# Optimization experiments

Measured on AMD Instinct MI355X. Metric: run time of the kernel, lower is better.

Reference implementation:

```python
import jax, jax.numpy as jnp
import numpy as np

N_BINS = 15


def setup_inputs() -> dict:
    key = jax.random.key(0)
    k1, k2 = jax.random.split(key)
    B, C = 4, 4
    spatial = (128, 128, 128)
    logits = jax.random.normal(k1, (B, C) + spatial, dtype=jnp.float32)
    labels = jax.random.randint(k2, (B, 1) + spatial, 0, C, dtype=jnp.int64)
    return {"logits": logits, "labels": labels}


def _hl1_ace(logits, labels, n_bins=N_BINS):
    B, C = logits.shape[0], logits.shape[1]
    probs = jax.nn.softmax(logits, axis=1) if C > 1 else logits
    # one-hot target (B, C, *spatial)
    target = jax.nn.one_hot(labels[:, 0], C, axis=1, dtype=jnp.float32)
    p = probs.reshape(B, C, -1).astype(jnp.float32)   # (B, C, N)
    t = target.reshape(B, C, -1)                       # (B, C, N)

    eps = jnp.finfo(jnp.float32).eps
    boundaries = jnp.linspace(0.0, 1.0 + eps, n_bins + 1)
    # torch.bucketize(p, boundaries[1:], right=False) == searchsorted side='left'
    bin_idx = jnp.searchsorted(boundaries[1:], p, side="left")  # (B, C, N)

    # fused histogram across all (b, c) slices via one segment_sum
    offsets = (jnp.arange(B * C, dtype=bin_idx.dtype) * n_bins).reshape(B, C, 1)
    seg = (bin_idx + offsets).reshape(-1)
    nseg = B * C * n_bins
    counts = jax.ops.segment_sum(jnp.ones(seg.shape, jnp.float32), seg, num_segments=nseg).reshape(B, C, n_bins)
    sum_p = jax.ops.segment_sum(p.reshape(-1), seg, num_segments=nseg).reshape(B, C, n_bins)
    sum_t = jax.ops.segment_sum(t.reshape(-1), seg, num_segments=nseg).reshape(B, C, n_bins)

    valid = counts > 0
    denom = jnp.where(valid, counts, 1.0)
    mean_p = sum_p / denom
    mean_t = sum_t / denom
    # nanmean over bins: average |mean_p - mean_t| over non-empty bins only
    diff = jnp.where(valid, jnp.abs(mean_p - mean_t), 0.0)
    n_valid = jnp.maximum(valid.sum(-1), 1)
    ace_per_bc = diff.sum(-1) / n_valid.astype(jnp.float32)  # (B, C)

    non_empty = (t.sum(-1) > 0).astype(jnp.float32)          # (B, C)
    return (ace_per_bc * non_empty).mean()


def reference(logits, labels):
    return _hl1_ace(logits, labels)
```

## Files before the change

### kernel.cpp

```cpp
#include <hip/hip_runtime.h>

#define NVOX 2097152u
#define NBINS 15
#define NSEG 240

#if __has_builtin(__builtin_amdgcn_exp2f)
#define EXP2F(x) __builtin_amdgcn_exp2f(x)
#else
#define EXP2F(x) exp2f(x)
#endif
#if __has_builtin(__builtin_amdgcn_rcpf)
#define RCPF(x) __builtin_amdgcn_rcpf(x)
#else
#define RCPF(x) (1.0f / (x))
#endif

__global__ __launch_bounds__(256)
void ace_zero(unsigned* __restrict__ ws) {
    int i = blockIdx.x * 256 + threadIdx.x;
    if (i < 3 * NSEG) ws[i] = 0u;
}

__global__ __launch_bounds__(256, 8)
void ace_hist(const float* __restrict__ logits,
              const int*   __restrict__ labels,
              unsigned* __restrict__ g_cnt,
              unsigned* __restrict__ g_cntt,
              float*    __restrict__ g_sump)
{
    __shared__ unsigned s_hist[60][64];
    __shared__ unsigned s_tab[3][60];

    const int tid  = threadIdx.x;
    const int lane = tid & 63;

    #pragma unroll
    for (int i = 0; i < 15; ++i) ((unsigned*)s_hist)[tid + i * 256] = 0u;
    if (tid < 180) ((unsigned*)s_tab)[tid] = 0u;
    __syncthreads();

    const unsigned b   = (unsigned)blockIdx.x >> 9;
    const unsigned tib = ((unsigned)blockIdx.x & 511u) * 256u + (unsigned)tid;

    const float step  = (1.0f + 1.1920929e-7f) / 15.0f;
    const float scale = 15.0f / (1.0f + 1.1920929e-7f);
    const float LOG2E = 1.44269504088896340736f;

    const float* lbase   = logits + (unsigned long long)(b * 4u) * NVOX;
    const int*   labbase = labels + (unsigned long long)b * NVOX;

    for (int i = 0; i < 4; ++i) {
        const unsigned s = (tib + (unsigned)i * 131072u) << 2;

        const int4 lv4 = *(const int4*)(labbase + s);
        const int lab[4] = { lv4.x, lv4.y, lv4.z, lv4.w };

        const float4 L0 = *(const float4*)(lbase + s);
        const float4 L1 = *(const float4*)(lbase + NVOX + s);
        const float4 L2 = *(const float4*)(lbase + 2u * NVOX + s);
        const float4 L3 = *(const float4*)(lbase + 3u * NVOX + s);

        #pragma unroll
        for (int v = 0; v < 4; ++v) {
            const float e0 = EXP2F((&L0.x)[v] * LOG2E);
            const float e1 = EXP2F((&L1.x)[v] * LOG2E);
            const float e2 = EXP2F((&L2.x)[v] * LOG2E);
            const float e3 = EXP2F((&L3.x)[v] * LOG2E);
            const float inv = RCPF(e0 + e1 + e2 + e3);
            const float pr[4] = { e0 * inv, e1 * inv, e2 * inv, e3 * inv };
            const int lv = lab[v];

            #pragma unroll
            for (int c = 0; c < 4; ++c) {
                const float pv = pr[c];
                int bin = (int)(pv * scale);
                bin = bin > 14 ? 14 : bin;
                if (bin < 14 && step * (float)(bin + 1) < pv) ++bin;
                if (bin > 0 && !(step * (float)bin < pv)) --bin;

                const unsigned qt  = (unsigned)fmaf(pv, 4095.0f, 262144.5f);
                const unsigned inc = qt | ((lv == c) ? 0x2000000u : 0u);
                atomicAdd(&s_hist[c * NBINS + bin][lane], inc);
            }
        }
    }
    __syncthreads();

    if (tid < 240) {
        const int r = tid >> 2, q = tid & 3;
        unsigned sq = 0, sc = 0, st = 0;
        #pragma unroll
        for (int j = 0; j < 16; ++j) {
            const unsigned x = s_hist[r][q * 16 + ((j + r) & 15)];
            sq += x & 0x3FFFFu;
            sc += (x >> 18) & 0x7Fu;
            st += x >> 25;
        }
        atomicAdd(&s_tab[0][r], sq);
        atomicAdd(&s_tab[1][r], sc);
        atomicAdd(&s_tab[2][r], st);
    }
    __syncthreads();

    if (tid < 60) {
        const int gi = (int)(b * 60u) + tid;
        atomicAdd(g_cnt  + gi, s_tab[1][tid]);
        atomicAdd(g_cntt + gi, s_tab[2][tid]);
        atomicAdd(g_sump + gi, (float)s_tab[0][tid] * (1.0f / 4095.0f));
    }
}

__global__ __launch_bounds__(64)
void ace_final(const unsigned* __restrict__ g_cnt,
               const unsigned* __restrict__ g_cntt,
               const float*    __restrict__ g_sump,
               float* __restrict__ out)
{
    const int lane = threadIdx.x;
    float contrib = 0.0f;
    if (lane < 16) {
        float diff_sum = 0.0f;
        int   nvalid   = 0;
        unsigned tot_t = 0u;
        for (int k = 0; k < NBINS; ++k) {
            const int i = lane * NBINS + k;
            const unsigned c  = g_cnt[i];
            const unsigned ct = g_cntt[i];
            const float    sp = g_sump[i];
            tot_t += ct;
            if (c > 0u) {
                const float invc = 1.0f / (float)c;
                diff_sum += fabsf(sp * invc - (float)ct * invc);
                ++nvalid;
            }
        }
        const float ace = diff_sum / (float)(nvalid > 0 ? nvalid : 1);
        contrib = (tot_t > 0u) ? ace : 0.0f;
    }
    #pragma unroll
    for (int off = 32; off > 0; off >>= 1)
        contrib += __shfl_xor(contrib, off, 64);
    if (lane == 0) out[0] = contrib * (1.0f / 16.0f);
}

extern "C" void kernel_launch(void* const* d_in, const int* in_sizes, int n_in,
                              void* d_out, int out_size, void* d_ws, size_t ws_size,
                              hipStream_t stream) {
    const float* logits = (const float*)d_in[0];
    const int*   labels = (const int*)d_in[1];

    unsigned* g_cnt  = (unsigned*)d_ws;
    unsigned* g_cntt = g_cnt + NSEG;
    float*    g_sump = (float*)(g_cntt + NSEG);
    float*    out    = (float*)d_out;

    ace_zero<<<3, 256, 0, stream>>>((unsigned*)d_ws);
    ace_hist<<<2048, 256, 0, stream>>>(logits, labels, g_cnt, g_cntt, g_sump);
    ace_final<<<1, 64, 0, stream>>>(g_cnt, g_cntt, g_sump, out);
}
```

Before: 55.50 us.

## Issue all loads up front per thread and drop exact bin boundary correction

Each thread now handles 16 contiguous voxels, with every label and logit float4 load issued before any compute. This raises memory-level parallelism, and the launch bound drops to 4 waves per SIMD to leave room for the extra registers. The boundary fix-up that matched searchsorted exactly is removed, so binning relies only on truncating p*scale. That can misbin values sitting on a boundary, and the contiguous per-thread layout changes the coalescing pattern.

New measurement: 56.69 us. +2.1%, slower.

```diff
diff --git a/kernel.cpp b/kernel.cpp
--- a/kernel.cpp
+++ b/kernel.cpp
@@ -21,7 +21,38 @@
     if (i < 3 * NSEG) ws[i] = 0u;
 }
 
-__global__ __launch_bounds__(256, 8)
+__device__ __forceinline__ void process4(const int4 lv4,
+                                         const float4 L0, const float4 L1,
+                                         const float4 L2, const float4 L3,
+                                         unsigned (*s_hist)[64], const int lane)
+{
+    const float scale = 15.0f / (1.0f + 1.1920929e-7f);
+    const float LOG2E = 1.44269504088896340736f;
+    const int lab[4] = { lv4.x, lv4.y, lv4.z, lv4.w };
+
+    #pragma unroll
+    for (int v = 0; v < 4; ++v) {
+        const float e0 = EXP2F((&L0.x)[v] * LOG2E);
+        const float e1 = EXP2F((&L1.x)[v] * LOG2E);
+        const float e2 = EXP2F((&L2.x)[v] * LOG2E);
+        const float e3 = EXP2F((&L3.x)[v] * LOG2E);
+        const float inv = RCPF(e0 + e1 + e2 + e3);
+        const float pr[4] = { e0 * inv, e1 * inv, e2 * inv, e3 * inv };
+        const int lv = lab[v];
+
+        #pragma unroll
+        for (int c = 0; c < 4; ++c) {
+            const float pv = pr[c];
+            const int bin = (int)(pv * scale);
+
+            const unsigned qt  = (unsigned)fmaf(pv, 4095.0f, 262144.5f);
+            const unsigned inc = qt | ((lv == c) ? 0x2000000u : 0u);
+            atomicAdd(&s_hist[c * NBINS + bin][lane], inc);
+        }
+    }
+}
+
+__global__ __launch_bounds__(256, 4)
 void ace_hist(const float* __restrict__ logits,
               const int*   __restrict__ labels,
               unsigned* __restrict__ g_cnt,
@@ -41,49 +72,29 @@
 
     const unsigned b   = (unsigned)blockIdx.x >> 9;
     const unsigned tib = ((unsigned)blockIdx.x & 511u) * 256u + (unsigned)tid;
+    const unsigned v0  = tib << 4;
 
-    const float step  = (1.0f + 1.1920929e-7f) / 15.0f;
-    const float scale = 15.0f / (1.0f + 1.1920929e-7f);
-    const float LOG2E = 1.44269504088896340736f;
+    const float* p0 = logits + (unsigned long long)(b * 4u) * NVOX + v0;
+    const int*   ap = labels + (unsigned long long)b * NVOX + v0;
 
-    const float* lbase   = logits + (unsigned long long)(b * 4u) * NVOX;
-    const int*   labbase = labels + (unsigned long long)b * NVOX;
+    int4 lv[4];
+    #pragma unroll
+    for (int j = 0; j < 4; ++j) lv[j] = *(const int4*)(ap + 4 * j);
 
-    for (int i = 0; i < 4; ++i) {
-        const unsigned s = (tib + (unsigned)i * 131072u) << 2;
+    float4 L0[4], L1[4], L2[4], L3[4];
+    #pragma unroll
+    for (int j = 0; j < 4; ++j) L0[j] = *(const float4*)(p0 + 4 * j);
+    #pragma unroll
+    for (int j = 0; j < 4; ++j) L1[j] = *(const float4*)(p0 + NVOX + 4 * j);
+    #pragma unroll
+    for (int j = 0; j < 4; ++j) L2[j] = *(const float4*)(p0 + 2u * NVOX + 4 * j);
+    #pragma unroll
+    for (int j = 0; j < 4; ++j) L3[j] = *(const float4*)(p0 + 3u * NVOX + 4 * j);
 
-        const int4 lv4 = *(const int4*)(labbase + s);
-        const int lab[4] = { lv4.x, lv4.y, lv4.z, lv4.w };
+    #pragma unroll
+    for (int j = 0; j < 4; ++j)
+        process4(lv[j], L0[j], L1[j], L2[j], L3[j], s_hist, lane);
 
-        const float4 L0 = *(const float4*)(lbase + s);
-        const float4 L1 = *(const float4*)(lbase + NVOX + s);
-        const float4 L2 = *(const float4*)(lbase + 2u * NVOX + s);
-        const float4 L3 = *(const float4*)(lbase + 3u * NVOX + s);
-
-        #pragma unroll
-        for (int v = 0; v < 4; ++v) {
-            const float e0 = EXP2F((&L0.x)[v] * LOG2E);
-            const float e1 = EXP2F((&L1.x)[v] * LOG2E);
-            const float e2 = EXP2F((&L2.x)[v] * LOG2E);
-            const float e3 = EXP2F((&L3.x)[v] * LOG2E);
-            const float inv = RCPF(e0 + e1 + e2 + e3);
-            const float pr[4] = { e0 * inv, e1 * inv, e2 * inv, e3 * inv };
-            const int lv = lab[v];
-
-            #pragma unroll
-            for (int c = 0; c < 4; ++c) {
-                const float pv = pr[c];
-                int bin = (int)(pv * scale);
-                bin = bin > 14 ? 14 : bin;
-                if (bin < 14 && step * (float)(bin + 1) < pv) ++bin;
-                if (bin > 0 && !(step * (float)bin < pv)) --bin;
-
-                const unsigned qt  = (unsigned)fmaf(pv, 4095.0f, 262144.5f);
-                const unsigned inc = qt | ((lv == c) ? 0x2000000u : 0u);
-                atomicAdd(&s_hist[c * NBINS + bin][lane], inc);
-            }
-        }
-    }
     __syncthreads();
 
     if (tid < 240) {
```
